# Performance work log

Measured on AMD Instinct MI355X. Metric: run time of the kernel, lower is better.

The kernel has to match this reference:

```python
import jax, jax.numpy as jnp
import numpy as np

# AlphaFold-style dims; n_seq must equal seq_len due to the source's bias broadcast
C_M, C_Z, C_H, N_H = 256, 128, 32, 8
B, N_SEQ, L = 1, 256, 256
LN_EPS = 1e-5


def _ln(x, g, b):
    mu = jnp.mean(x, axis=-1, keepdims=True)
    var = jnp.mean(jnp.square(x - mu), axis=-1, keepdims=True)
    return (x - mu) * jax.lax.rsqrt(var + LN_EPS) * g + b


def setup_inputs() -> dict:
    key = jax.random.key(0)
    ks = jax.random.split(key, 8)
    s = 0.02
    return {
        "m": jax.random.normal(ks[0], (B, N_SEQ, L, C_M), jnp.float32),
        "z": jax.random.normal(ks[1], (B, L, L, C_Z), jnp.float32),
        "g_m": jnp.ones((C_M,), jnp.float32),
        "b_m": jnp.zeros((C_M,), jnp.float32),
        "g_z": jnp.ones((C_Z,), jnp.float32),
        "b_z": jnp.zeros((C_Z,), jnp.float32),
        "Wq": jax.random.normal(ks[2], (C_M, N_H * C_H), jnp.float32) * s,
        "Wk": jax.random.normal(ks[3], (C_M, N_H * C_H), jnp.float32) * s,
        "Wv": jax.random.normal(ks[4], (C_M, N_H * C_H), jnp.float32) * s,
        "Wb": jax.random.normal(ks[5], (C_Z, N_H), jnp.float32) * s,
        "Wg": jax.random.normal(ks[6], (C_M, N_H * C_H), jnp.float32) * s,
        "bg": jnp.zeros((N_H * C_H,), jnp.float32),
        "Wo": jax.random.normal(ks[7], (N_H * C_H, C_M), jnp.float32) * s,
        "bo": jnp.zeros((C_M,), jnp.float32),
    }


def reference(m, z, g_m, b_m, g_z, b_z, Wq, Wk, Wv, Wb, Wg, bg, Wo, bo):
    b_, s_, l_, _ = m.shape
    m_ln = _ln(m, g_m, b_m)          # [B,S,L,c_m]
    z_ln = _ln(z, g_z, b_z)          # [B,L,L,c_z]
    # project and permute to [B, L, H, S, c] exactly as the torch source does
    def proj(W):
        return (m_ln @ W).reshape(b_, s_, l_, N_H, C_H).transpose(0, 2, 3, 1, 4)
    q, k, v = proj(Wq), proj(Wk), proj(Wv)
    # pair bias: [B,H,L,L] -> [B,1,H,L,L]
    bias = jnp.einsum('bijz,zh->bhij', z_ln, Wb)[:, None]
    inv_sqrt_c = np.float32(1.0 / np.sqrt(C_H))
    logits = jnp.einsum('blhsc,blhtc->blhst', q, k) * inv_sqrt_c + bias  # [B,L,H,S,S]
    w = jax.nn.softmax(logits, axis=-1)
    o = jnp.einsum('blhst,blhtc->blhsc', w, v)          # [B,L,H,S,c]
    o = o.transpose(0, 3, 1, 2, 4).reshape(b_, s_, l_, N_H * C_H)  # [B,S,L,H*c]
    g = jax.nn.sigmoid(m_ln @ Wg + bg)
    return (g * o) @ Wo + bo
```

## Files before the change

### kernel.cpp

```cpp
#include <hip/hip_runtime.h>
#include <cstdint>
#include <cstddef>

using bfrag8 = __attribute__((ext_vector_type(8))) short;
using facc4  = __attribute__((ext_vector_type(4))) float;

__device__ __forceinline__ unsigned short f2bf(float f){
  unsigned int u = __builtin_bit_cast(unsigned int, f);
  u += 0x7fffu + ((u >> 16) & 1u);
  return (unsigned short)(u >> 16);
}
__device__ __forceinline__ float bf2f(unsigned short h){
  unsigned int u = ((unsigned int)h) << 16;
  return __builtin_bit_cast(float, u);
}
__device__ __forceinline__ unsigned int pk2(float a, float b){
  return (unsigned int)f2bf(a) | ((unsigned int)f2bf(b) << 16);
}
__device__ __forceinline__ facc4 mm16(bfrag8 a, bfrag8 b, facc4 c){
  return __builtin_amdgcn_mfma_f32_16x16x32_bf16(a, b, c, 0, 0, 0);
}

__global__ __launch_bounds__(256) void kp_prep(
    const float* __restrict__ Wq, const float* __restrict__ Wk,
    const float* __restrict__ Wv, const float* __restrict__ Wg,
    const float* __restrict__ Wo, unsigned short* __restrict__ WT){
  int b = blockIdx.x;
  int w = b >> 8;
  int k = b & 255;
  int n = threadIdx.x;
  const float* W = (w==0)?Wq:(w==1)?Wk:(w==2)?Wv:(w==3)?Wg:Wo;
  int kk = (w == 4) ? ((k & ~31) | ((k & 15) << 1) | ((k >> 4) & 1)) : k;
  WT[w*65536 + n*256 + kk] = f2bf(W[k*256 + n]);
}

__global__ __launch_bounds__(256, 4) void kp_proj(
    const float* __restrict__ m, const float* __restrict__ g_m,
    const float* __restrict__ b_m, const unsigned short* __restrict__ WT,
    const float* __restrict__ bg,
    unsigned short* __restrict__ qws, unsigned short* __restrict__ kws,
    unsigned short* __restrict__ vws, unsigned short* __restrict__ gws){
  __shared__ __align__(16) char smem[45056];
  unsigned short* Mt = (unsigned short*)smem;
  int tid = threadIdx.x;
  int l   = blockIdx.x & 255;
  int s0b = (blockIdx.x >> 8) * 64;

  for (int iter = 0; iter < 2; iter++){
    int rw = iter*32 + (tid >> 3);
    int part = tid & 7;
    const float* mrow = m + ((size_t)((s0b + rw)*256 + l))*256 + part*32;
    float x[32];
    float s1 = 0.f, s2 = 0.f;
#pragma unroll
    for (int j = 0; j < 8; j++){
      float4 v = reinterpret_cast<const float4*>(mrow)[j];
      x[j*4+0]=v.x; x[j*4+1]=v.y; x[j*4+2]=v.z; x[j*4+3]=v.w;
      s1 += v.x+v.y+v.z+v.w;
      s2 += v.x*v.x+v.y*v.y+v.z*v.z+v.w*v.w;
    }
    s1 += __shfl_xor(s1,1); s1 += __shfl_xor(s1,2); s1 += __shfl_xor(s1,4);
    s2 += __shfl_xor(s2,1); s2 += __shfl_xor(s2,2); s2 += __shfl_xor(s2,4);
    float mu = s1*(1.f/256.f);
    float var = s2*(1.f/256.f) - mu*mu;
    float rs = rsqrtf(var + 1e-5f);
    const float* gmp = g_m + part*32;
    const float* bmp = b_m + part*32;
#pragma unroll
    for (int c4 = 0; c4 < 4; c4++){
      bfrag8 st;
#pragma unroll
      for (int e = 0; e < 8; e++){
        int kk = c4*8+e;
        float y = (x[kk]-mu)*rs*gmp[kk] + bmp[kk];
        st[e] = (short)f2bf(y);
      }
      int c = part*4 + c4;
      *reinterpret_cast<bfrag8*>(&Mt[rw*256 + ((c ^ (rw & 7)) << 3)]) = st;
    }
  }
  __syncthreads();

  int w = tid >> 6, lane = tid & 63, i = lane & 15, g = lane >> 4;
  char* EW = smem + 32768 + w*3072;

#pragma unroll 1
  for (int wi = 0; wi < 4; wi++){
    const unsigned short* WTw = WT + wi*65536;
    facc4 acc[4][4];
#pragma unroll
    for (int mt = 0; mt < 4; mt++)
#pragma unroll
      for (int nt = 0; nt < 4; nt++)
        acc[mt][nt] = (facc4){0.f,0.f,0.f,0.f};
#pragma unroll 2
    for (int ks = 0; ks < 8; ks++){
      bfrag8 a[4];
#pragma unroll
      for (int mt = 0; mt < 4; mt++)
        a[mt] = *reinterpret_cast<const bfrag8*>(
            &Mt[(mt*16+i)*256 + (((ks*4+g) ^ (i & 7)) << 3)]);
#pragma unroll
      for (int nt = 0; nt < 4; nt++){
        bfrag8 b = *reinterpret_cast<const bfrag8*>(
            WTw + (w*64 + nt*16 + i)*256 + ks*32 + g*8);
#pragma unroll
        for (int mt = 0; mt < 4; mt++)
          acc[mt][nt] = mm16(a[mt], b, acc[mt][nt]);
      }
    }

    if (wi < 2){
      unsigned short* dst = (wi == 0) ? qws : kws;
#pragma unroll 1
      for (int mt = 0; mt < 4; mt++){
#pragma unroll
        for (int r = 0; r < 4; r++){
          *reinterpret_cast<unsigned int*>(EW + (4*g+r)*144 + i*4)
              = pk2(acc[mt][0][r], acc[mt][1][r]);
          *reinterpret_cast<unsigned int*>(EW + (4*g+r)*144 + 64 + i*4)
              = pk2(acc[mt][2][r], acc[mt][3][r]);
        }
#pragma unroll
        for (int rd = 0; rd < 2; rd++){
          int rw2 = rd*8 + (lane >> 3), ch = lane & 7;
          uint4 vv = *reinterpret_cast<uint4*>(EW + rw2*144 + ch*16);
          int ss = s0b + mt*16 + rw2;
          int hh = w*2 + (ch >> 2);
          *reinterpret_cast<uint4*>((char*)dst +
              ((size_t)(((l*8+hh)*256 + ss)*32 + (ch&3)*8))*2) = vv;
        }
      }
    } else if (wi == 2){
#pragma unroll 1
      for (int mt = 0; mt < 4; mt++){
#pragma unroll
        for (int nt = 0; nt < 4; nt++){
          uint2 vv;
          vv.x = pk2(acc[mt][nt][0], acc[mt][nt][1]);
          vv.y = pk2(acc[mt][nt][2], acc[mt][nt][3]);
          *reinterpret_cast<uint2*>(EW + (nt*16+i)*48 + g*8) = vv;
        }
        int c = lane;
        int hh = w*2 + (c >> 5), cc = c & 31;
        uint4 a0 = *reinterpret_cast<uint4*>(EW + c*48);
        uint4 a1 = *reinterpret_cast<uint4*>(EW + c*48 + 16);
        size_t eo = ((size_t)((l*8+hh)*32 + cc))*256 + s0b + mt*16;
        *reinterpret_cast<uint4*>((char*)vws + eo*2)      = a0;
        *reinterpret_cast<uint4*>((char*)vws + eo*2 + 16) = a1;
      }
    } else {
      float bgv0 = bg[w*64 + i],      bgv1 = bg[w*64 + 16 + i];
      float bgv2 = bg[w*64 + 32 + i], bgv3 = bg[w*64 + 48 + i];
#pragma unroll 1
      for (int mt = 0; mt < 4; mt++){
#pragma unroll
        for (int r = 0; r < 4; r++){
          float t0 = acc[mt][0][r] + bgv0, t1 = acc[mt][1][r] + bgv1;
          float t2 = acc[mt][2][r] + bgv2, t3 = acc[mt][3][r] + bgv3;
          t0 = 1.f/(1.f+__expf(-t0)); t1 = 1.f/(1.f+__expf(-t1));
          t2 = 1.f/(1.f+__expf(-t2)); t3 = 1.f/(1.f+__expf(-t3));
          *reinterpret_cast<unsigned int*>(EW + (4*g+r)*144 + i*4)      = pk2(t0, t1);
          *reinterpret_cast<unsigned int*>(EW + (4*g+r)*144 + 64 + i*4) = pk2(t2, t3);
        }
#pragma unroll
        for (int rd = 0; rd < 2; rd++){
          int rw2 = rd*8 + (lane >> 3), ch = lane & 7;
          uint4 vv = *reinterpret_cast<uint4*>(EW + rw2*144 + ch*16);
          int grow = (s0b + mt*16 + rw2)*256 + l;
          *reinterpret_cast<uint4*>((char*)gws +
              ((size_t)grow*256 + w*64 + ch*8)*2) = vv;
        }
      }
    }
  }
}

__global__ __launch_bounds__(256, 4) void kp_bias(
    const float* __restrict__ z, const float* __restrict__ g_z,
    const float* __restrict__ b_z, const float* __restrict__ Wb,
    unsigned short* __restrict__ biasT){
  __shared__ float WbL[128*8];
  __shared__ float gzL[128], bzL[128];
  int tid = threadIdx.x;
  for (int t = tid; t < 1024; t += 256) WbL[t] = Wb[t];
  if (tid < 128){ gzL[tid] = g_z[tid]; bzL[tid] = b_z[tid]; }
  __syncthreads();

  int grow = blockIdx.x*64 + (tid >> 2);
  int part = tid & 3;
  const float* zr = z + (size_t)grow*128 + part*32;
  float x[32];
  float s1 = 0.f, s2 = 0.f;
#pragma unroll
  for (int j = 0; j < 8; j++){
    float4 v = reinterpret_cast<const float4*>(zr)[j];
    x[j*4+0]=v.x; x[j*4+1]=v.y; x[j*4+2]=v.z; x[j*4+3]=v.w;
    s1 += v.x+v.y+v.z+v.w;
    s2 += v.x*v.x+v.y*v.y+v.z*v.z+v.w*v.w;
  }
  s1 += __shfl_xor(s1,1); s1 += __shfl_xor(s1,2);
  s2 += __shfl_xor(s2,1); s2 += __shfl_xor(s2,2);
  float mu = s1*(1.f/128.f);
  float var = s2*(1.f/128.f) - mu*mu;
  float rs = rsqrtf(var + 1e-5f);
  float acc[8] = {0,0,0,0,0,0,0,0};
#pragma unroll
  for (int zi = 0; zi < 32; zi++){
    int zl = part*32 + zi;
    float v = (x[zi]-mu)*rs*gzL[zl] + bzL[zl];
    float4 wa = *reinterpret_cast<const float4*>(&WbL[zl*8]);
    float4 wb = *reinterpret_cast<const float4*>(&WbL[zl*8+4]);
    acc[0] += v*wa.x; acc[1] += v*wa.y; acc[2] += v*wa.z; acc[3] += v*wa.w;
    acc[4] += v*wb.x; acc[5] += v*wb.y; acc[6] += v*wb.z; acc[7] += v*wb.w;
  }
#pragma unroll
  for (int hh = 0; hh < 8; hh++){
    acc[hh] += __shfl_xor(acc[hh],1);
    acc[hh] += __shfl_xor(acc[hh],2);
  }
  const float ISC = 5.656854249492381f;
  float v0, v1;
  if      (part == 0){ v0 = acc[0]; v1 = acc[1]; }
  else if (part == 1){ v0 = acc[2]; v1 = acc[3]; }
  else if (part == 2){ v0 = acc[4]; v1 = acc[5]; }
  else               { v0 = acc[6]; v1 = acc[7]; }
  biasT[(2*part)*65536 + grow]   = f2bf(v0*ISC);
  biasT[(2*part+1)*65536 + grow] = f2bf(v1*ISC);
}

__global__ __launch_bounds__(256, 4) void kp_attn(
    const unsigned short* __restrict__ qws, const unsigned short* __restrict__ kws,
    const unsigned short* __restrict__ vws, const unsigned short* __restrict__ biasT,
    unsigned short* __restrict__ ows){
  __shared__ __align__(16) char smem[49152];
  char* VtB = smem;
  int tid = threadIdx.x;
  int bid = blockIdx.x;
  int l = bid >> 3, h = bid & 7;
  int base = bid * 8192;

#pragma unroll
  for (int it = 0; it < 4; it++){
    int f = tid + it*256;
    int c = f >> 5, sc = f & 31;
    bfrag8 v = *reinterpret_cast<const bfrag8*>(vws + base + f*8);
    *reinterpret_cast<bfrag8*>(VtB + ((c*512 + sc*16) ^ ((c & 7) << 4))) = v;
  }
  __syncthreads();

  int w = tid >> 6, lane = tid & 63, i = lane & 15, g = lane >> 4;
  char* PtW = smem + 16384 + w*8192;
  const int swzi = (i & 7) << 4;
  const float SC = 0.17677669529663689f;
  const unsigned short* bb = biasT + h*65536;

#pragma unroll 1
  for (int pass = 0; pass < 4; pass++){
    int s0 = (pass*4 + w)*16;
    bfrag8 qf = *reinterpret_cast<const bfrag8*>(qws + base + (s0+i)*32 + g*8);
    facc4 accs[16];
#pragma unroll
    for (int tt = 0; tt < 16; tt++){
      bfrag8 kf = *reinterpret_cast<const bfrag8*>(kws + base + (tt*16+i)*32 + g*8);
      uint2 bv = *reinterpret_cast<const uint2*>(bb + (s0+i)*256 + tt*16 + 4*g);
      facc4 c;
      c[0] = bf2f((unsigned short)(bv.x));
      c[1] = bf2f((unsigned short)(bv.x >> 16));
      c[2] = bf2f((unsigned short)(bv.y));
      c[3] = bf2f((unsigned short)(bv.y >> 16));
      accs[tt] = mm16(kf, qf, c);
    }
    float mx = -3.0e38f;
#pragma unroll
    for (int tt = 0; tt < 16; tt++){
      float m2 = fmaxf(fmaxf(accs[tt][0], accs[tt][1]),
                       fmaxf(accs[tt][2], accs[tt][3]));
      mx = fmaxf(mx, m2);
    }
    mx = fmaxf(mx, __shfl_xor(mx, 16));
    mx = fmaxf(mx, __shfl_xor(mx, 32));
    float sum = 0.f;
#pragma unroll
    for (int tt = 0; tt < 16; tt++){
      float p0 = __expf((accs[tt][0]-mx)*SC);
      float p1 = __expf((accs[tt][1]-mx)*SC);
      float p2 = __expf((accs[tt][2]-mx)*SC);
      float p3 = __expf((accs[tt][3]-mx)*SC);
      sum += (p0+p1) + (p2+p3);
      uint2 pv; pv.x = pk2(p0,p1); pv.y = pk2(p2,p3);
      *reinterpret_cast<uint2*>(PtW + ((i*512 + tt*32 + g*8) ^ swzi)) = pv;
    }
    sum += __shfl_xor(sum, 16);
    sum += __shfl_xor(sum, 32);
    float invRow = 1.0f / sum;
    facc4 o0 = (facc4){0.f,0.f,0.f,0.f}, o1 = (facc4){0.f,0.f,0.f,0.f};
#pragma unroll 2
    for (int kt = 0; kt < 8; kt++){
      bfrag8 pa = *reinterpret_cast<const bfrag8*>(
          PtW + ((i*512 + kt*64 + g*16) ^ swzi));
      bfrag8 b0 = *reinterpret_cast<const bfrag8*>(
          VtB + ((i*512 + kt*64 + g*16) ^ ((i & 7) << 4)));
      bfrag8 b1 = *reinterpret_cast<const bfrag8*>(
          VtB + (((16+i)*512 + kt*64 + g*16) ^ ((i & 7) << 4)));
      o0 = mm16(pa, b0, o0);
      o1 = mm16(pa, b1, o1);
    }
#pragma unroll
    for (int r = 0; r < 4; r++){
      float invr = __shfl(invRow, (g << 4) + (g << 2) + r);
      *reinterpret_cast<unsigned int*>(PtW + (4*g+r)*80 + i*4)
          = pk2(o0[r]*invr, o1[r]*invr);
    }
    {
      int row = lane >> 2, ch = lane & 3;
      uint4 ov = *reinterpret_cast<uint4*>(PtW + row*80 + ch*16);
      *reinterpret_cast<uint4*>((char*)ows +
          (((size_t)(s0+row)*256 + l)*256 + h*32 + ch*8)*2) = ov;
    }
  }
}

__global__ __launch_bounds__(256, 4) void kp_out(
    const unsigned short* __restrict__ gws, const unsigned short* __restrict__ ows,
    const unsigned short* __restrict__ WT, const float* __restrict__ bo,
    float* __restrict__ out){
  __shared__ __align__(16) unsigned short Mt[64*256];
  int tid = threadIdx.x;
  int r0  = blockIdx.x * 64;
  {
    int rw = tid >> 2, part = tid & 3;
    int grow = r0 + rw;
    const unsigned short* gp = gws + (size_t)grow*256 + part*64;
    const unsigned short* op = ows + (size_t)grow*256 + part*64;
#pragma unroll
    for (int c8 = 0; c8 < 8; c8++){
      bfrag8 gv = *reinterpret_cast<const bfrag8*>(gp + c8*8);
      bfrag8 ov = *reinterpret_cast<const bfrag8*>(op + c8*8);
      bfrag8 st;
#pragma unroll
      for (int e = 0; e < 8; e++){
        float y = bf2f((unsigned short)gv[e]) * bf2f((unsigned short)ov[e]);
        st[e] = (short)f2bf(y);
      }
      int c = part*8 + c8;
      *reinterpret_cast<bfrag8*>(&Mt[rw*256 + ((c ^ (rw & 7)) << 3)]) = st;
    }
  }
  __syncthreads();

  int w = tid >> 6, lane = tid & 63, i = lane & 15, g = lane >> 4;
  const unsigned short* WTw = WT + 4*65536;
  facc4 acc[4][4];
#pragma unroll
  for (int mt = 0; mt < 4; mt++)
#pragma unroll
    for (int nt = 0; nt < 4; nt++)
      acc[mt][nt] = (facc4){0.f,0.f,0.f,0.f};
#pragma unroll 2
  for (int ks = 0; ks < 8; ks++){
    bfrag8 a[4];
#pragma unroll
    for (int mt = 0; mt < 4; mt++)
      a[mt] = *reinterpret_cast<const bfrag8*>(
          &Mt[(mt*16+i)*256 + (((ks*4+g) ^ (i & 7)) << 3)]);
#pragma unroll
    for (int nt = 0; nt < 4; nt++){
      bfrag8 b = *reinterpret_cast<const bfrag8*>(
          WTw + (w*64 + nt*16 + i)*256 + ks*32 + g*8);
#pragma unroll
      for (int mt = 0; mt < 4; mt++)
        acc[mt][nt] = mm16(a[mt], b, acc[mt][nt]);
    }
  }
#pragma unroll
  for (int nt = 0; nt < 4; nt++){
    int col = w*64 + nt*16 + i;
    float bov = bo[col];
#pragma unroll
    for (int mt = 0; mt < 4; mt++){
#pragma unroll
      for (int r = 0; r < 4; r++){
        int grow = r0 + mt*16 + 4*g + r;
        out[(size_t)grow*256 + col] = acc[mt][nt][r] + bov;
      }
    }
  }
}

extern "C" void kernel_launch(void* const* d_in, const int* in_sizes, int n_in,
                              void* d_out, int out_size, void* d_ws, size_t ws_size,
                              hipStream_t stream) {
  (void)in_sizes; (void)n_in; (void)out_size; (void)ws_size;
  const float* m   = (const float*)d_in[0];
  const float* z   = (const float*)d_in[1];
  const float* g_m = (const float*)d_in[2];
  const float* b_m = (const float*)d_in[3];
  const float* g_z = (const float*)d_in[4];
  const float* b_z = (const float*)d_in[5];
  const float* Wq  = (const float*)d_in[6];
  const float* Wk  = (const float*)d_in[7];
  const float* Wv  = (const float*)d_in[8];
  const float* Wb  = (const float*)d_in[9];
  const float* Wg  = (const float*)d_in[10];
  const float* bg  = (const float*)d_in[11];
  const float* Wo  = (const float*)d_in[12];
  const float* bo  = (const float*)d_in[13];

  char* ws = (char*)d_ws;
  unsigned short* qws    = (unsigned short*)(ws);
  unsigned short* kws    = (unsigned short*)(ws + 33554432);
  unsigned short* vws    = (unsigned short*)(ws + 67108864);
  unsigned short* gws    = (unsigned short*)(ws + 100663296);
  unsigned short* ows    = (unsigned short*)(ws + 134217728);
  unsigned short* biasT  = (unsigned short*)(ws + 167772160);
  unsigned short* WT     = (unsigned short*)(ws + 168820736);
  float* out = (float*)d_out;

  kp_prep<<<dim3(1280), dim3(256), 0, stream>>>(Wq, Wk, Wv, Wg, Wo, WT);
  kp_proj<<<dim3(1024), dim3(256), 0, stream>>>(m, g_m, b_m, WT, bg, qws, kws, vws, gws);
  kp_bias<<<dim3(1024), dim3(256), 0, stream>>>(z, g_z, b_z, Wb, biasT);
  kp_attn<<<dim3(2048), dim3(256), 0, stream>>>(qws, kws, vws, biasT, ows);
  kp_out <<<dim3(1024), dim3(256), 0, stream>>>(gws, ows, WT, bo, out);
}
```

Before: 471.8 us.

## Fuse QKV projection into attention and gate projection into output kernel

Replaces the separate projection kernel with a LayerNorm-only kernel that writes a transposed bf16 m_ln buffer. The attention kernel now computes Q, K and V for its (l, h) tile directly from m_ln with MFMA and keeps them in shared memory. The output kernel computes the sigmoid gate from m_ln, multiplies it by the attention output and then applies Wo. This removes the large Q/K/V/G workspace round-trips through HBM. In exchange, the QKV projection is recomputed per head from 256-wide m_ln rows, shared memory use rises, and occupancy drops to 2 blocks per CU.

```diff
diff --git a/kernel.cpp b/kernel.cpp
--- a/kernel.cpp
+++ b/kernel.cpp
@@ -30,149 +30,55 @@
   int k = b & 255;
   int n = threadIdx.x;
   const float* W = (w==0)?Wq:(w==1)?Wk:(w==2)?Wv:(w==3)?Wg:Wo;
-  int kk = (w == 4) ? ((k & ~31) | ((k & 15) << 1) | ((k >> 4) & 1)) : k;
-  WT[w*65536 + n*256 + kk] = f2bf(W[k*256 + n]);
-}
-
-__global__ __launch_bounds__(256, 4) void kp_proj(
+  int kk = k, nn = n;
+  if (w == 4) kk = (k & ~31) | ((k & 15) << 1) | ((k >> 4) & 1);
+  if (w == 3) nn = (n & ~31) | ((n & 15) << 1) | ((n >> 4) & 1);
+  WT[w*65536 + nn*256 + kk] = f2bf(W[k*256 + n]);
+}
+
+__global__ __launch_bounds__(256) void kp_ln(
     const float* __restrict__ m, const float* __restrict__ g_m,
-    const float* __restrict__ b_m, const unsigned short* __restrict__ WT,
-    const float* __restrict__ bg,
-    unsigned short* __restrict__ qws, unsigned short* __restrict__ kws,
-    unsigned short* __restrict__ vws, unsigned short* __restrict__ gws){
-  __shared__ __align__(16) char smem[45056];
-  unsigned short* Mt = (unsigned short*)smem;
+    const float* __restrict__ b_m, unsigned short* __restrict__ mln){
+  __shared__ __align__(16) unsigned short T[32*256];
   int tid = threadIdx.x;
-  int l   = blockIdx.x & 255;
-  int s0b = (blockIdx.x >> 8) * 64;
-
-  for (int iter = 0; iter < 2; iter++){
-    int rw = iter*32 + (tid >> 3);
-    int part = tid & 7;
-    const float* mrow = m + ((size_t)((s0b + rw)*256 + l))*256 + part*32;
-    float x[32];
-    float s1 = 0.f, s2 = 0.f;
-#pragma unroll
-    for (int j = 0; j < 8; j++){
-      float4 v = reinterpret_cast<const float4*>(mrow)[j];
-      x[j*4+0]=v.x; x[j*4+1]=v.y; x[j*4+2]=v.z; x[j*4+3]=v.w;
-      s1 += v.x+v.y+v.z+v.w;
-      s2 += v.x*v.x+v.y*v.y+v.z*v.z+v.w*v.w;
-    }
-    s1 += __shfl_xor(s1,1); s1 += __shfl_xor(s1,2); s1 += __shfl_xor(s1,4);
-    s2 += __shfl_xor(s2,1); s2 += __shfl_xor(s2,2); s2 += __shfl_xor(s2,4);
-    float mu = s1*(1.f/256.f);
-    float var = s2*(1.f/256.f) - mu*mu;
-    float rs = rsqrtf(var + 1e-5f);
-    const float* gmp = g_m + part*32;
-    const float* bmp = b_m + part*32;
-#pragma unroll
-    for (int c4 = 0; c4 < 4; c4++){
-      bfrag8 st;
-#pragma unroll
-      for (int e = 0; e < 8; e++){
-        int kk = c4*8+e;
-        float y = (x[kk]-mu)*rs*gmp[kk] + bmp[kk];
-        st[e] = (short)f2bf(y);
-      }
-      int c = part*4 + c4;
-      *reinterpret_cast<bfrag8*>(&Mt[rw*256 + ((c ^ (rw & 7)) << 3)]) = st;
-    }
-  }
-  __syncthreads();
-
-  int w = tid >> 6, lane = tid & 63, i = lane & 15, g = lane >> 4;
-  char* EW = smem + 32768 + w*3072;
-
-#pragma unroll 1
-  for (int wi = 0; wi < 4; wi++){
-    const unsigned short* WTw = WT + wi*65536;
-    facc4 acc[4][4];
-#pragma unroll
-    for (int mt = 0; mt < 4; mt++)
-#pragma unroll
-      for (int nt = 0; nt < 4; nt++)
-        acc[mt][nt] = (facc4){0.f,0.f,0.f,0.f};
-#pragma unroll 2
-    for (int ks = 0; ks < 8; ks++){
-      bfrag8 a[4];
-#pragma unroll
-      for (int mt = 0; mt < 4; mt++)
-        a[mt] = *reinterpret_cast<const bfrag8*>(
-            &Mt[(mt*16+i)*256 + (((ks*4+g) ^ (i & 7)) << 3)]);
-#pragma unroll
-      for (int nt = 0; nt < 4; nt++){
-        bfrag8 b = *reinterpret_cast<const bfrag8*>(
-            WTw + (w*64 + nt*16 + i)*256 + ks*32 + g*8);
-#pragma unroll
-        for (int mt = 0; mt < 4; mt++)
-          acc[mt][nt] = mm16(a[mt], b, acc[mt][nt]);
-      }
-    }
-
-    if (wi < 2){
-      unsigned short* dst = (wi == 0) ? qws : kws;
-#pragma unroll 1
-      for (int mt = 0; mt < 4; mt++){
-#pragma unroll
-        for (int r = 0; r < 4; r++){
-          *reinterpret_cast<unsigned int*>(EW + (4*g+r)*144 + i*4)
-              = pk2(acc[mt][0][r], acc[mt][1][r]);
-          *reinterpret_cast<unsigned int*>(EW + (4*g+r)*144 + 64 + i*4)
-              = pk2(acc[mt][2][r], acc[mt][3][r]);
-        }
-#pragma unroll
-        for (int rd = 0; rd < 2; rd++){
-          int rw2 = rd*8 + (lane >> 3), ch = lane & 7;
-          uint4 vv = *reinterpret_cast<uint4*>(EW + rw2*144 + ch*16);
-          int ss = s0b + mt*16 + rw2;
-          int hh = w*2 + (ch >> 2);
-          *reinterpret_cast<uint4*>((char*)dst +
-              ((size_t)(((l*8+hh)*256 + ss)*32 + (ch&3)*8))*2) = vv;
-        }
-      }
-    } else if (wi == 2){
-#pragma unroll 1
-      for (int mt = 0; mt < 4; mt++){
-#pragma unroll
-        for (int nt = 0; nt < 4; nt++){
-          uint2 vv;
-          vv.x = pk2(acc[mt][nt][0], acc[mt][nt][1]);
-          vv.y = pk2(acc[mt][nt][2], acc[mt][nt][3]);
-          *reinterpret_cast<uint2*>(EW + (nt*16+i)*48 + g*8) = vv;
-        }
-        int c = lane;
-        int hh = w*2 + (c >> 5), cc = c & 31;
-        uint4 a0 = *reinterpret_cast<uint4*>(EW + c*48);
-        uint4 a1 = *reinterpret_cast<uint4*>(EW + c*48 + 16);
-        size_t eo = ((size_t)((l*8+hh)*32 + cc))*256 + s0b + mt*16;
-        *reinterpret_cast<uint4*>((char*)vws + eo*2)      = a0;
-        *reinterpret_cast<uint4*>((char*)vws + eo*2 + 16) = a1;
-      }
-    } else {
-      float bgv0 = bg[w*64 + i],      bgv1 = bg[w*64 + 16 + i];
-      float bgv2 = bg[w*64 + 32 + i], bgv3 = bg[w*64 + 48 + i];
-#pragma unroll 1
-      for (int mt = 0; mt < 4; mt++){
-#pragma unroll
-        for (int r = 0; r < 4; r++){
-          float t0 = acc[mt][0][r] + bgv0, t1 = acc[mt][1][r] + bgv1;
-          float t2 = acc[mt][2][r] + bgv2, t3 = acc[mt][3][r] + bgv3;
-          t0 = 1.f/(1.f+__expf(-t0)); t1 = 1.f/(1.f+__expf(-t1));
-          t2 = 1.f/(1.f+__expf(-t2)); t3 = 1.f/(1.f+__expf(-t3));
-          *reinterpret_cast<unsigned int*>(EW + (4*g+r)*144 + i*4)      = pk2(t0, t1);
-          *reinterpret_cast<unsigned int*>(EW + (4*g+r)*144 + 64 + i*4) = pk2(t2, t3);
-        }
-#pragma unroll
-        for (int rd = 0; rd < 2; rd++){
-          int rw2 = rd*8 + (lane >> 3), ch = lane & 7;
-          uint4 vv = *reinterpret_cast<uint4*>(EW + rw2*144 + ch*16);
-          int grow = (s0b + mt*16 + rw2)*256 + l;
-          *reinterpret_cast<uint4*>((char*)gws +
-              ((size_t)grow*256 + w*64 + ch*8)*2) = vv;
-        }
-      }
-    }
+  int r0 = blockIdx.x * 32;
+  int rowL = tid >> 3, part = tid & 7;
+  int rowg = r0 + rowL;
+  const float* mrow = m + (size_t)rowg*256 + part*32;
+  float x[32];
+  float s1 = 0.f, s2 = 0.f;
+#pragma unroll
+  for (int j = 0; j < 8; j++){
+    float4 v = reinterpret_cast<const float4*>(mrow)[j];
+    x[j*4+0]=v.x; x[j*4+1]=v.y; x[j*4+2]=v.z; x[j*4+3]=v.w;
+    s1 += v.x+v.y+v.z+v.w;
+    s2 += v.x*v.x+v.y*v.y+v.z*v.z+v.w*v.w;
+  }
+  s1 += __shfl_xor(s1,1); s1 += __shfl_xor(s1,2); s1 += __shfl_xor(s1,4);
+  s2 += __shfl_xor(s2,1); s2 += __shfl_xor(s2,2); s2 += __shfl_xor(s2,4);
+  float mu = s1*(1.f/256.f);
+  float var = s2*(1.f/256.f) - mu*mu;
+  float rs = rsqrtf(var + 1e-5f);
+  const float* gmp = g_m + part*32;
+  const float* bmp = b_m + part*32;
+#pragma unroll
+  for (int c4 = 0; c4 < 4; c4++){
+    bfrag8 st;
+#pragma unroll
+    for (int e = 0; e < 8; e++){
+      int kk = c4*8+e;
+      float y = (x[kk]-mu)*rs*gmp[kk] + bmp[kk];
+      st[e] = (short)f2bf(y);
+    }
+    *reinterpret_cast<bfrag8*>(&T[rowL*256 + part*32 + c4*8]) = st;
+  }
+  __syncthreads();
+  int s = rowg >> 8, l = rowg & 255;
+  unsigned short* dst = mln + ((size_t)(l*256 + s))*256;
+#pragma unroll
+  for (int j = 0; j < 4; j++){
+    bfrag8 v = *reinterpret_cast<const bfrag8*>(&T[rowL*256 + j*64 + part*8]);
+    *reinterpret_cast<bfrag8*>(dst + j*64 + part*8) = v;
   }
 }
 
@@ -229,28 +135,98 @@
   biasT[(2*part+1)*65536 + grow] = f2bf(v1*ISC);
 }
 
-__global__ __launch_bounds__(256, 4) void kp_attn(
-    const unsigned short* __restrict__ qws, const unsigned short* __restrict__ kws,
-    const unsigned short* __restrict__ vws, const unsigned short* __restrict__ biasT,
-    unsigned short* __restrict__ ows){
-  __shared__ __align__(16) char smem[49152];
-  char* VtB = smem;
+__global__ __launch_bounds__(256, 2) void kp_attn2(
+    const unsigned short* __restrict__ mln, const unsigned short* __restrict__ WT,
+    const unsigned short* __restrict__ biasT, unsigned short* __restrict__ ows){
+  __shared__ __align__(16) char smem[81920];
+  unsigned short* qT = (unsigned short*)smem;
+  unsigned short* kT = (unsigned short*)(smem+16384);
+  char* vTB = smem + 32768;
+  char* PAN = smem + 49152;
+
   int tid = threadIdx.x;
   int bid = blockIdx.x;
-  int l = bid >> 3, h = bid & 7;
-  int base = bid * 8192;
-
-#pragma unroll
-  for (int it = 0; it < 4; it++){
-    int f = tid + it*256;
-    int c = f >> 5, sc = f & 31;
-    bfrag8 v = *reinterpret_cast<const bfrag8*>(vws + base + f*8);
-    *reinterpret_cast<bfrag8*>(VtB + ((c*512 + sc*16) ^ ((c & 7) << 4))) = v;
-  }
-  __syncthreads();
+  int slot = bid & 7, idx = bid >> 3;
+  int h = idx & 7;
+  int l = slot + ((idx >> 3) << 3);
 
   int w = tid >> 6, lane = tid & 63, i = lane & 15, g = lane >> 4;
-  char* PtW = smem + 16384 + w*8192;
+
+  const unsigned short* WQ = WT + 0*65536 + (h*32)*256;
+  const unsigned short* WK = WT + 1*65536 + (h*32)*256;
+  const unsigned short* WV = WT + 2*65536 + (h*32)*256;
+  facc4 aq[4][2], ak[4][2], av[4][2];
+#pragma unroll
+  for (int mt = 0; mt < 4; mt++)
+#pragma unroll
+    for (int nt = 0; nt < 2; nt++){
+      aq[mt][nt] = (facc4){0.f,0.f,0.f,0.f};
+      ak[mt][nt] = (facc4){0.f,0.f,0.f,0.f};
+      av[mt][nt] = (facc4){0.f,0.f,0.f,0.f};
+    }
+
+#pragma unroll 1
+  for (int kp = 0; kp < 4; kp++){
+    __syncthreads();
+#pragma unroll
+    for (int it = 0; it < 8; it++){
+      int cid = it*256 + tid;
+      int s = cid >> 3, kc = cid & 7;
+      bfrag8 v = *reinterpret_cast<const bfrag8*>(
+          mln + ((size_t)(l*256 + s))*256 + kp*64 + kc*8);
+      *reinterpret_cast<bfrag8*>(PAN + s*128 + ((kc ^ (s & 7)) << 4)) = v;
+    }
+    __syncthreads();
+#pragma unroll
+    for (int ksub = 0; ksub < 2; ksub++){
+      int kglob = kp*64 + ksub*32;
+      bfrag8 bq0 = *reinterpret_cast<const bfrag8*>(WQ + i*256        + kglob + g*8);
+      bfrag8 bq1 = *reinterpret_cast<const bfrag8*>(WQ + (16+i)*256   + kglob + g*8);
+      bfrag8 bk0 = *reinterpret_cast<const bfrag8*>(WK + i*256        + kglob + g*8);
+      bfrag8 bk1 = *reinterpret_cast<const bfrag8*>(WK + (16+i)*256   + kglob + g*8);
+      bfrag8 bv0 = *reinterpret_cast<const bfrag8*>(WV + i*256        + kglob + g*8);
+      bfrag8 bv1 = *reinterpret_cast<const bfrag8*>(WV + (16+i)*256   + kglob + g*8);
+#pragma unroll
+      for (int mt = 0; mt < 4; mt++){
+        int row = w*64 + mt*16 + i;
+        bfrag8 a = *reinterpret_cast<const bfrag8*>(
+            PAN + row*128 + ((((ksub<<2)+g) ^ (row & 7)) << 4));
+        aq[mt][0] = mm16(a, bq0, aq[mt][0]);
+        aq[mt][1] = mm16(a, bq1, aq[mt][1]);
+        ak[mt][0] = mm16(a, bk0, ak[mt][0]);
+        ak[mt][1] = mm16(a, bk1, ak[mt][1]);
+        av[mt][0] = mm16(a, bv0, av[mt][0]);
+        av[mt][1] = mm16(a, bv1, av[mt][1]);
+      }
+    }
+  }
+
+#pragma unroll
+  for (int mt = 0; mt < 4; mt++){
+#pragma unroll
+    for (int r = 0; r < 4; r++){
+      int s = w*64 + mt*16 + 4*g + r;
+      int sw = (((i >> 2) ^ ((s >> 1) & 3)) << 4) + (i & 3)*4;
+      *reinterpret_cast<unsigned int*>((char*)qT + s*64 + sw)
+          = pk2(aq[mt][0][r], aq[mt][1][r]);
+      *reinterpret_cast<unsigned int*>((char*)kT + s*64 + sw)
+          = pk2(ak[mt][0][r], ak[mt][1][r]);
+    }
+#pragma unroll
+    for (int nt = 0; nt < 2; nt++){
+      int c = nt*16 + i;
+      int t0 = w*64 + mt*16 + 4*g;
+      uint2 vv;
+      vv.x = pk2(av[mt][nt][0], av[mt][nt][1]);
+      vv.y = pk2(av[mt][nt][2], av[mt][nt][3]);
+      int tc = t0 >> 3;
+      int half = (t0 >> 2) & 1;
+      *reinterpret_cast<uint2*>(vTB + c*512 + ((tc ^ (c & 7)) << 4) + half*8) = vv;
+    }
+  }
+  __syncthreads();
+
+  char* PtW = PAN + w*8192;
   const int swzi = (i & 7) << 4;
   const float SC = 0.17677669529663689f;
   const unsigned short* bb = biasT + h*65536;
@@ -258,11 +234,15 @@
 #pragma unroll 1
   for (int pass = 0; pass < 4; pass++){
     int s0 = (pass*4 + w)*16;
-    bfrag8 qf = *reinterpret_cast<const bfrag8*>(qws + base + (s0+i)*32 + g*8);
+    int qs = s0 + i;
+    bfrag8 qf = *reinterpret_cast<const bfrag8*>(
+        (char*)qT + qs*64 + ((g ^ ((qs >> 1) & 3)) << 4));
     facc4 accs[16];
 #pragma unroll
     for (int tt = 0; tt < 16; tt++){
-      bfrag8 kf = *reinterpret_cast<const bfrag8*>(kws + base + (tt*16+i)*32 + g*8);
+      int t = tt*16 + i;
+      bfrag8 kf = *reinterpret_cast<const bfrag8*>(
+          (char*)kT + t*64 + ((g ^ ((t >> 1) & 3)) << 4));
       uint2 bv = *reinterpret_cast<const uint2*>(bb + (s0+i)*256 + tt*16 + 4*g);
       facc4 c;
       c[0] = bf2f((unsigned short)(bv.x));
@@ -299,10 +279,11 @@
     for (int kt = 0; kt < 8; kt++){
       bfrag8 pa = *reinterpret_cast<const bfrag8*>(
           PtW + ((i*512 + kt*64 + g*16) ^ swzi));
+      int tc = kt*4 + g;
       bfrag8 b0 = *reinterpret_cast<const bfrag8*>(
-          VtB + ((i*512 + kt*64 + g*16) ^ ((i & 7) << 4)));
+          vTB + i*512 + ((tc ^ (i & 7)) << 4));
       bfrag8 b1 = *reinterpret_cast<const bfrag8*>(
-          VtB + (((16+i)*512 + kt*64 + g*16) ^ ((i & 7) << 4)));
+          vTB + (16+i)*512 + ((tc ^ (i & 7)) << 4));
       o0 = mm16(pa, b0, o0);
       o1 = mm16(pa, b1, o1);
     }
@@ -321,36 +302,34 @@
   }
 }
 
-__global__ __launch_bounds__(256, 4) void kp_out(
-    const unsigned short* __restrict__ gws, const unsigned short* __restrict__ ows,
-    const unsigned short* __restrict__ WT, const float* __restrict__ bo,
-    float* __restrict__ out){
-  __shared__ __align__(16) unsigned short Mt[64*256];
+__global__ __launch_bounds__(256, 2) void kp_out2(
+    const unsigned short* __restrict__ mln, const unsigned short* __restrict__ ows,
+    const unsigned short* __restrict__ WT, const float* __restrict__ bg,
+    const float* __restrict__ bo, float* __restrict__ out){
+  __shared__ __align__(16) char smem[65536];
+  char* Mt = smem;
+  char* Ot = smem + 32768;
   int tid = threadIdx.x;
   int r0  = blockIdx.x * 64;
-  {
-    int rw = tid >> 2, part = tid & 3;
-    int grow = r0 + rw;
-    const unsigned short* gp = gws + (size_t)grow*256 + part*64;
-    const unsigned short* op = ows + (size_t)grow*256 + part*64;
-#pragma unroll
-    for (int c8 = 0; c8 < 8; c8++){
-      bfrag8 gv = *reinterpret_cast<const bfrag8*>(gp + c8*8);
-      bfrag8 ov = *reinterpret_cast<const bfrag8*>(op + c8*8);
-      bfrag8 st;
-#pragma unroll
-      for (int e = 0; e < 8; e++){
-        float y = bf2f((unsigned short)gv[e]) * bf2f((unsigned short)ov[e]);
-        st[e] = (short)f2bf(y);
-      }
-      int c = part*8 + c8;
-      *reinterpret_cast<bfrag8*>(&Mt[rw*256 + ((c ^ (rw & 7)) << 3)]) = st;
-    }
+  int s   = r0 >> 8, l0 = r0 & 255;
+
+#pragma unroll
+  for (int it = 0; it < 8; it++){
+    int cid = it*256 + tid;
+    int rowL = cid >> 5, ch = cid & 31;
+    bfrag8 a = *reinterpret_cast<const bfrag8*>(
+        mln + ((size_t)((l0+rowL)*256 + s))*256 + ch*8);
+    *reinterpret_cast<bfrag8*>(Mt + rowL*512 + ((ch ^ (rowL & 7)) << 4)) = a;
+    bfrag8 b = *reinterpret_cast<const bfrag8*>(
+        ows + (size_t)(r0+rowL)*256 + ch*8);
+    *reinterpret_cast<bfrag8*>(Ot + rowL*512 + ((ch ^ (rowL & 7)) << 4)) = b;
   }
   __syncthreads();
 
   int w = tid >> 6, lane = tid & 63, i = lane & 15, g = lane >> 4;
-  const unsigned short* WTw = WT + 4*65536;
+  const unsigned short* WTg = WT + 3*65536;
+  const unsigned short* WTo = WT + 4*65536;
+
   facc4 acc[4][4];
 #pragma unroll
   for (int mt = 0; mt < 4; mt++)
@@ -361,16 +340,69 @@
   for (int ks = 0; ks < 8; ks++){
     bfrag8 a[4];
 #pragma unroll
-    for (int mt = 0; mt < 4; mt++)
+    for (int mt = 0; mt < 4; mt++){
+      int row = mt*16 + i;
       a[mt] = *reinterpret_cast<const bfrag8*>(
-          &Mt[(mt*16+i)*256 + (((ks*4+g) ^ (i & 7)) << 3)]);
+          Mt + row*512 + ((((ks*4+g) ^ (row & 7))) << 4));
+    }
 #pragma unroll
     for (int nt = 0; nt < 4; nt++){
       bfrag8 b = *reinterpret_cast<const bfrag8*>(
-          WTw + (w*64 + nt*16 + i)*256 + ks*32 + g*8);
+          WTg + (w*64 + nt*16 + i)*256 + ks*32 + g*8);
 #pragma unroll
       for (int mt = 0; mt < 4; mt++)
         acc[mt][nt] = mm16(a[mt], b, acc[mt][nt]);
+    }
+  }
+
+  float bgv[4];
+#pragma unroll
+  for (int nt = 0; nt < 4; nt++){
+    int p = w*64 + nt*16 + i;
+    int ntr = (p & ~31) | ((p & 1) << 4) | ((p & 31) >> 1);
+    bgv[nt] = bg[ntr];
+  }
+  __syncthreads();
+#pragma unroll
+  for (int mt = 0; mt < 4; mt++){
+#pragma unroll
+    for (int nt = 0; nt < 4; nt++){
+      int p = w*64 + nt*16 + i;
+#pragma unroll
+      for (int r = 0; r < 4; r++){
+        int row = mt*16 + 4*g + r;
+        int off = row*512 + ((((p>>3) ^ (row & 7))) << 4) + (p & 7)*2;
+        float ov = bf2f(*reinterpret_cast<const unsigned short*>(Ot + off));
+        float t = acc[mt][nt][r] + bgv[nt];
+        float gg = 1.0f / (1.0f + __expf(-t));
+        *reinterpret_cast<unsigned short*>(Mt + off) = f2bf(gg * ov);
+      }
+    }
+  }
+  __syncthreads();
+
+  facc4 acc2[4][4];
+#pragma unroll
+  for (int mt = 0; mt < 4; mt++)
+#pragma unroll
+    for (int nt = 0; nt < 4; nt++)
+      acc2[mt][nt] = (facc4){0.f,0.f,0.f,0.f};
+#pragma unroll 2
+  for (int ks = 0; ks < 8; ks++){
+    bfrag8 a[4];
+#pragma unroll
+    for (int mt = 0; mt < 4; mt++){
+      int row = mt*16 + i;
+      a[mt] = *reinterpret_cast<const bfrag8*>(
+          Mt + row*512 + ((((ks*4+g) ^ (row & 7))) << 4));
+    }
+#pragma unroll
+    for (int nt = 0; nt < 4; nt++){
+      bfrag8 b = *reinterpret_cast<const bfrag8*>(
+          WTo + (w*64 + nt*16 + i)*256 + ks*32 + g*8);
+#pragma unroll
+      for (int mt = 0; mt < 4; mt++)
+        acc2[mt][nt] = mm16(a[mt], b, acc2[mt][nt]);
     }
   }
 #pragma unroll
@@ -382,7 +414,7 @@
 #pragma unroll
       for (int r = 0; r < 4; r++){
         int grow = r0 + mt*16 + 4*g + r;
-        out[(size_t)grow*256 + col] = acc[mt][nt][r] + bov;
+        out[(size_t)grow*256 + col] = acc2[mt][nt][r] + bov;
       }
     }
   }
@@ -408,18 +440,15 @@
   const float* bo  = (const float*)d_in[13];
 
   char* ws = (char*)d_ws;
-  unsigned short* qws    = (unsigned short*)(ws);
-  unsigned short* kws    = (unsigned short*)(ws + 33554432);
-  unsigned short* vws    = (unsigned short*)(ws + 67108864);
-  unsigned short* gws    = (unsigned short*)(ws + 100663296);
-  unsigned short* ows    = (unsigned short*)(ws + 134217728);
-  unsigned short* biasT  = (unsigned short*)(ws + 167772160);
-  unsigned short* WT     = (unsigned short*)(ws + 168820736);
+  unsigned short* mln    = (unsigned short*)(ws);
+  unsigned short* ows    = (unsigned short*)(ws + 33554432);
+  unsigned short* biasT  = (unsigned short*)(ws + 67108864);
+  unsigned short* WT     = (unsigned short*)(ws + 68157440);
   float* out = (float*)d_out;
 
-  kp_prep<<<dim3(1280), dim3(256), 0, stream>>>(Wq, Wk, Wv, Wg, Wo, WT);
-  kp_proj<<<dim3(1024), dim3(256), 0, stream>>>(m, g_m, b_m, WT, bg, qws, kws, vws, gws);
-  kp_bias<<<dim3(1024), dim3(256), 0, stream>>>(z, g_z, b_z, Wb, biasT);
-  kp_attn<<<dim3(2048), dim3(256), 0, stream>>>(qws, kws, vws, biasT, ows);
-  kp_out <<<dim3(1024), dim3(256), 0, stream>>>(gws, ows, WT, bo, out);
-}
+  kp_prep <<<dim3(1280), dim3(256), 0, stream>>>(Wq, Wk, Wv, Wg, Wo, WT);
+  kp_ln   <<<dim3(2048), dim3(256), 0, stream>>>(m, g_m, b_m, mln);
+  kp_bias <<<dim3(1024), dim3(256), 0, stream>>>(z, g_z, b_z, Wb, biasT);
+  kp_attn2<<<dim3(2048), dim3(256), 0, stream>>>(mln, WT, biasT, ows);
+  kp_out2 <<<dim3(1024), dim3(256), 0, stream>>>(mln, ows, WT, bg, bo, out);
+}
```

After: 379.9 us. 19.5% less time.
